# Kernel optimization log

Hardware: AMD Instinct MI355X
Metric: run time of the kernel (lower is better)

The kernel has to match this reference:

```python
import jax, jax.numpy as jnp
import numpy as np

# init_kwargs baked in as constants
OUTPUT_TYPE = "all"   # one of 'class', 'box', 'all'
CONF = 0.25
RATIO = 0.25
N = 1_000_000
C = 80


def setup_inputs() -> dict:
    key = jax.random.key(0)
    k1, k2 = jax.random.split(key)
    logits = jax.random.normal(k1, (N, C), dtype=jnp.float32)
    boxes = jax.random.uniform(k2, (N, 4), dtype=jnp.float32)
    return {"logits": logits, "boxes": boxes}


def reference(logits, boxes):
    # Number of top rows to consider (rows assumed pre-sorted by confidence).
    n = logits.shape[0]
    k = max(1, int(n * RATIO)) if n > 0 else 0

    # Row-wise max class score over the first k rows: [k]
    scores = jnp.max(logits[:k], axis=1)

    # The torch loop breaks at the FIRST score < conf. Vectorized: keep[i] = 1
    # iff all scores[0..i] >= conf (cumulative AND as a cumprod of 0/1).
    keep = jnp.cumprod((scores >= CONF).astype(logits.dtype))  # [k]

    total = jnp.zeros((), dtype=logits.dtype)
    if OUTPUT_TYPE in ("class", "all"):
        total = total + jnp.sum(keep * scores)
    if OUTPUT_TYPE in ("box", "all"):
        # targets.extend(boxes[i]) sums all 4 coords of each kept row.
        total = total + jnp.sum(keep[:, None] * boxes[:k])
    # If nothing is kept, keep is all zeros and total == 0.0, matching the
    # torch fallback return of tensor(0.0).
    return total
```

## Files before the change

### kernel.cpp

```cpp
#include <hip/hip_runtime.h>
#include <math.h>

#define CONF 0.25f
#define NCLS 80

__global__ void init_kernel(unsigned int* __restrict__ first_fail, unsigned int k) {
    *first_fail = k;
}

__global__ __launch_bounds__(256) void score_kernel(
    const float* __restrict__ logits,
    const float* __restrict__ boxes,
    float* __restrict__ scores,
    float* __restrict__ boxsum,
    unsigned int* __restrict__ first_fail,
    unsigned int k)
{
    const int tid   = threadIdx.x;
    const int lane4 = tid & 3;
    const int grp   = tid >> 2;
    const unsigned int row = blockIdx.x * 64u + (unsigned int)grp;
    if (row >= k) return;

    const float4* rp = (const float4*)(logits + (size_t)row * NCLS);
    float m = -INFINITY;
#pragma unroll
    for (int t = 0; t < 5; ++t) {
        float4 v = rp[lane4 + 4 * t];
        m = fmaxf(m, fmaxf(fmaxf(v.x, v.y), fmaxf(v.z, v.w)));
    }
    m = fmaxf(m, __shfl_xor(m, 1));
    m = fmaxf(m, __shfl_xor(m, 2));

    if (lane4 == 0) {
        scores[row] = m;
        float4 b = ((const float4*)boxes)[row];
        boxsum[row] = (b.x + b.y) + (b.z + b.w);
        if (m < CONF) atomicMin(first_fail, row);
    }
}

__global__ __launch_bounds__(256) void reduce_kernel(
    const float* __restrict__ scores,
    const float* __restrict__ boxsum,
    const unsigned int* __restrict__ first_fail,
    float* __restrict__ partials,
    unsigned int k)
{
    unsigned int j = *first_fail;
    if (j > k) j = k;

    float s = 0.0f;
    const unsigned int stride = gridDim.x * blockDim.x;
    for (unsigned int i = blockIdx.x * blockDim.x + threadIdx.x; i < j; i += stride)
        s += scores[i] + boxsum[i];

#pragma unroll
    for (int o = 32; o > 0; o >>= 1) s += __shfl_down(s, o);

    __shared__ float ls[4];
    const int lane = threadIdx.x & 63;
    const int wid  = threadIdx.x >> 6;
    if (lane == 0) ls[wid] = s;
    __syncthreads();
    if (threadIdx.x == 0)
        partials[blockIdx.x] = (ls[0] + ls[1]) + (ls[2] + ls[3]);
}

__global__ void final_kernel(const float* __restrict__ partials, float* __restrict__ out) {
    float s = partials[threadIdx.x] + partials[threadIdx.x + 64] +
              partials[threadIdx.x + 128] + partials[threadIdx.x + 192];
#pragma unroll
    for (int o = 32; o > 0; o >>= 1) s += __shfl_down(s, o);
    if (threadIdx.x == 0) out[0] = s;
}

extern "C" void kernel_launch(void* const* d_in, const int* in_sizes, int n_in,
                              void* d_out, int out_size, void* d_ws, size_t ws_size,
                              hipStream_t stream) {
    const float* logits = (const float*)d_in[0];
    const float* boxes  = (const float*)d_in[1];
    float* out = (float*)d_out;

    const unsigned int N = (unsigned int)(in_sizes[0] / NCLS);
    unsigned int k = N / 4;
    if (k < 1) k = 1;

    char* ws = (char*)d_ws;
    unsigned int* first_fail = (unsigned int*)ws;
    float* partials = (float*)(ws + 256);
    float* scores   = (float*)(ws + 4096);
    float* boxsum   = (float*)(ws + 4096 + (size_t)k * 4);

    init_kernel<<<1, 1, 0, stream>>>(first_fail, k);

    const unsigned int nb = (k + 63u) / 64u;
    score_kernel<<<nb, 256, 0, stream>>>(logits, boxes, scores, boxsum, first_fail, k);

    reduce_kernel<<<256, 256, 0, stream>>>(scores, boxsum, first_fail, partials, k);

    final_kernel<<<1, 64, 0, stream>>>(partials, out);
}
```

Baseline: 371.6 us.

## Fuse score, reduce and final kernels into single last-block-done pass

Merges the per-row max, the prefix-fail detection and the masked sum into one kernel. Each block writes a per-chunk sum and a per-chunk minimum fail row, and the last block to finish (found through an atomic counter) combines the chunk sums below the first failure, plus the partial chunk, from per-row values. This removes two kernel launches and the second pass over the scores and box-sum arrays. In exchange, the final reduction runs serially in a single block over about 3900 chunk entries, and correctness relies on threadfence ordering.

```diff
diff --git a/kernel.cpp b/kernel.cpp
--- a/kernel.cpp
+++ b/kernel.cpp
@@ -4,75 +4,103 @@
 #define CONF 0.25f
 #define NCLS 80
 
-__global__ void init_kernel(unsigned int* __restrict__ first_fail, unsigned int k) {
-    *first_fail = k;
+__global__ void yolo_init(unsigned int* __restrict__ done) {
+    *done = 0u;
 }
 
-__global__ __launch_bounds__(256) void score_kernel(
+__global__ __launch_bounds__(256) void yolo_fused(
     const float* __restrict__ logits,
     const float* __restrict__ boxes,
-    float* __restrict__ scores,
-    float* __restrict__ boxsum,
-    unsigned int* __restrict__ first_fail,
-    unsigned int k)
+    float* __restrict__ vrow,
+    float* __restrict__ chunksum,
+    unsigned int* __restrict__ chunkminfail,
+    unsigned int* __restrict__ done,
+    float* __restrict__ out,
+    unsigned int k, unsigned int nb)
 {
     const int tid   = threadIdx.x;
     const int lane4 = tid & 3;
     const int grp   = tid >> 2;
     const unsigned int row = blockIdx.x * 64u + (unsigned int)grp;
-    if (row >= k) return;
 
-    const float4* rp = (const float4*)(logits + (size_t)row * NCLS);
-    float m = -INFINITY;
+    float v = 0.0f;
+    unsigned int failrow = 0xFFFFFFFFu;
+
+    if (row < k) {
+        const float4* rp = (const float4*)(logits + (size_t)row * NCLS);
+        float m = -INFINITY;
 #pragma unroll
-    for (int t = 0; t < 5; ++t) {
-        float4 v = rp[lane4 + 4 * t];
-        m = fmaxf(m, fmaxf(fmaxf(v.x, v.y), fmaxf(v.z, v.w)));
+        for (int t = 0; t < 5; ++t) {
+            float4 c4 = rp[lane4 + 4 * t];
+            m = fmaxf(m, fmaxf(fmaxf(c4.x, c4.y), fmaxf(c4.z, c4.w)));
+        }
+        m = fmaxf(m, __shfl_xor(m, 1));
+        m = fmaxf(m, __shfl_xor(m, 2));
+
+        if (lane4 == 0) {
+            float4 b = ((const float4*)boxes)[row];
+            v = m + (b.x + b.y) + (b.z + b.w);
+            vrow[row] = v;
+            if (m < CONF) failrow = row;
+        }
     }
-    m = fmaxf(m, __shfl_xor(m, 1));
-    m = fmaxf(m, __shfl_xor(m, 2));
 
-    if (lane4 == 0) {
-        scores[row] = m;
-        float4 b = ((const float4*)boxes)[row];
-        boxsum[row] = (b.x + b.y) + (b.z + b.w);
-        if (m < CONF) atomicMin(first_fail, row);
+    float ws_v = v;
+    unsigned int wf = failrow;
+#pragma unroll
+    for (int o = 32; o > 0; o >>= 1) {
+        ws_v += __shfl_down(ws_v, o);
+        wf = min(wf, __shfl_down(wf, o));
     }
-}
 
-__global__ __launch_bounds__(256) void reduce_kernel(
-    const float* __restrict__ scores,
-    const float* __restrict__ boxsum,
-    const unsigned int* __restrict__ first_fail,
-    float* __restrict__ partials,
-    unsigned int k)
-{
-    unsigned int j = *first_fail;
+    __shared__ float        lsv[4];
+    __shared__ unsigned int lsf[4];
+    __shared__ unsigned int lsj[4];
+    __shared__ int islast;
+
+    const int lane = tid & 63;
+    const int wid  = tid >> 6;
+    if (lane == 0) { lsv[wid] = ws_v; lsf[wid] = wf; }
+    __syncthreads();
+
+    if (tid == 0) {
+        float cs        = (lsv[0] + lsv[1]) + (lsv[2] + lsv[3]);
+        unsigned int cf = min(min(lsf[0], lsf[1]), min(lsf[2], lsf[3]));
+        chunksum[blockIdx.x]     = cs;
+        chunkminfail[blockIdx.x] = cf;
+        __threadfence();
+        unsigned int t = atomicAdd(done, 1u);
+        islast = (t == nb - 1u);
+    }
+    __syncthreads();
+    if (!islast) return;
+
+    __threadfence();
+
+    unsigned int jmin = 0xFFFFFFFFu;
+    for (unsigned int c = (unsigned int)tid; c < nb; c += 256u)
+        jmin = min(jmin, chunkminfail[c]);
+#pragma unroll
+    for (int o = 32; o > 0; o >>= 1) jmin = min(jmin, __shfl_down(jmin, o));
+    if (lane == 0) lsj[wid] = jmin;
+    __syncthreads();
+    unsigned int j = min(min(lsj[0], lsj[1]), min(lsj[2], lsj[3]));
     if (j > k) j = k;
 
+    const unsigned int cfull = j >> 6;
     float s = 0.0f;
-    const unsigned int stride = gridDim.x * blockDim.x;
-    for (unsigned int i = blockIdx.x * blockDim.x + threadIdx.x; i < j; i += stride)
-        s += scores[i] + boxsum[i];
+    for (unsigned int c = (unsigned int)tid; c < cfull; c += 256u)
+        s += chunksum[c];
+    const unsigned int nbd = j & 63u;
+    if ((unsigned int)tid < nbd)
+        s += vrow[(size_t)cfull * 64u + (unsigned int)tid];
 
 #pragma unroll
     for (int o = 32; o > 0; o >>= 1) s += __shfl_down(s, o);
-
-    __shared__ float ls[4];
-    const int lane = threadIdx.x & 63;
-    const int wid  = threadIdx.x >> 6;
-    if (lane == 0) ls[wid] = s;
     __syncthreads();
-    if (threadIdx.x == 0)
-        partials[blockIdx.x] = (ls[0] + ls[1]) + (ls[2] + ls[3]);
-}
-
-__global__ void final_kernel(const float* __restrict__ partials, float* __restrict__ out) {
-    float s = partials[threadIdx.x] + partials[threadIdx.x + 64] +
-              partials[threadIdx.x + 128] + partials[threadIdx.x + 192];
-#pragma unroll
-    for (int o = 32; o > 0; o >>= 1) s += __shfl_down(s, o);
-    if (threadIdx.x == 0) out[0] = s;
+    if (lane == 0) lsv[wid] = s;
+    __syncthreads();
+    if (tid == 0) out[0] = (lsv[0] + lsv[1]) + (lsv[2] + lsv[3]);
 }
 
 extern "C" void kernel_launch(void* const* d_in, const int* in_sizes, int n_in,
@@ -85,19 +113,17 @@
     const unsigned int N = (unsigned int)(in_sizes[0] / NCLS);
     unsigned int k = N / 4;
     if (k < 1) k = 1;
+    const unsigned int nb = (k + 63u) / 64u;
 
     char* ws = (char*)d_ws;
-    unsigned int* first_fail = (unsigned int*)ws;
-    float* partials = (float*)(ws + 256);
-    float* scores   = (float*)(ws + 4096);
-    float* boxsum   = (float*)(ws + 4096 + (size_t)k * 4);
+    unsigned int* done = (unsigned int*)ws;
+    size_t off = 256;
+    unsigned int* cmf = (unsigned int*)(ws + off);
+    off += ((size_t)nb * 4 + 255) & ~(size_t)255;
+    float* csum = (float*)(ws + off);
+    off += ((size_t)nb * 4 + 255) & ~(size_t)255;
+    float* vrow = (float*)(ws + off);
 
-    init_kernel<<<1, 1, 0, stream>>>(first_fail, k);
-
-    const unsigned int nb = (k + 63u) / 64u;
-    score_kernel<<<nb, 256, 0, stream>>>(logits, boxes, scores, boxsum, first_fail, k);
-
-    reduce_kernel<<<256, 256, 0, stream>>>(scores, boxsum, first_fail, partials, k);
-
-    final_kernel<<<1, 64, 0, stream>>>(partials, out);
+    yolo_init<<<1, 1, 0, stream>>>(done);
+    yolo_fused<<<nb, 256, 0, stream>>>(logits, boxes, vrow, csum, cmf, done, out, k, nb);
 }
```

New measurement: 527.0 us. 1.42x slower.
